# Kernel optimization log

Measured on AMD Instinct MI355X. Metric: run time of the kernel, lower is better.

Reference implementation:

```python
import jax, jax.numpy as jnp
import numpy as np

H, W, C = 128, 128, 100
N_OBJ = 3
PAD_VAL = 1e20  # WRONG_LABEL_PADDING-style padding used by local_pairwise_distances2


def setup_inputs() -> dict:
    key = jax.random.key(0)
    k1, k2, k3 = jax.random.split(key, 3)
    return {
        "prev_frame_embedding": jax.random.normal(k1, (H, W, C), dtype=jnp.float32),
        "query_embedding": jax.random.normal(k2, (H, W, C), dtype=jnp.float32),
        "prev_frame_labels": jax.random.randint(k3, (H, W, 1), 0, N_OBJ),
        "gt_ids": jnp.arange(N_OBJ),
        "max_distance": 15,
    }


def _local_nn_features(query_embedding, prev_frame_embedding, prev_frame_labels, gt_ids, max_distance):
    h, w, c = query_embedding.shape
    k = 2 * max_distance + 1  # static python int -> static shapes
    n_obj = gt_ids.shape[0]

    # masks: [h, w, n_obj] -- labels are [h, w, 1], broadcast against gt_ids
    masks = prev_frame_labels == gt_ids[None, None, :]

    # pad reference embedding with a huge value (matches torch F.pad value=1e20),
    # pad masks with False (matches torch zero padding)
    y_pad = jnp.pad(prev_frame_embedding,
                    ((max_distance, max_distance), (max_distance, max_distance), (0, 0)),
                    constant_values=PAD_VAL)
    m_pad = jnp.pad(masks,
                    ((max_distance, max_distance), (max_distance, max_distance), (0, 0)))

    # offsets in the same order as the torch nested loops (y_start outer, x_start inner)
    offs = jnp.stack(jnp.meshgrid(jnp.arange(k), jnp.arange(k), indexing="ij"), -1).reshape(-1, 2)

    x = query_embedding

    def per_offset(off):
        y_sl = jax.lax.dynamic_slice(y_pad, (off[0], off[1], 0), (h, w, c))
        m_sl = jax.lax.dynamic_slice(m_pad, (off[0], off[1], 0), (h, w, n_obj))
        diff = x - y_sl
        d = jnp.sum(diff * diff, axis=-1)  # [h, w]
        return d, m_sl

    # sequential map over the k*k window offsets keeps peak memory small
    d, offset_masks = jax.lax.map(per_offset, offs)  # [k2,h,w], [k2,h,w,n_obj]
    d = jnp.transpose(d, (1, 2, 0))                   # [h, w, k2]
    offset_masks = jnp.transpose(offset_masks, (1, 2, 0, 3))  # [h, w, k2, n_obj]

    # mask out wrong-object / out-of-frame offsets with distance 1.0 (torch pad=ones_like)
    d_masked = jnp.where(offset_masks, d[..., None], jnp.float32(1.0))
    dists = jnp.min(d_masked, axis=2)  # [h, w, n_obj]
    return dists.reshape(1, h, w, n_obj, 1)


def reference(prev_frame_embedding, query_embedding, prev_frame_labels, gt_ids, max_distance):
    return _local_nn_features(query_embedding, prev_frame_embedding,
                              prev_frame_labels, gt_ids, max_distance)
```

## Files before the change

kernel.cpp:

```cpp
#include <hip/hip_runtime.h>
#include <cstdint>


#define HW   128
#define NC   100
#define MD   15
#define NOBJ 3
#define PIX  (HW * HW)
#define NOUT (PIX * NOBJ)
#define PEN_NM (1 << 22)
#define CSENT  (1 << 28)
#define IINIT  (1 << 30)

typedef __attribute__((ext_vector_type(4))) int intx4;

__device__ inline intx4 quant_pack16(const float* v) {
    signed char b[16];
#pragma unroll
    for (int j = 0; j < 16; ++j) {
        int qi = __float2int_rn(v[j] * 32.f);
        b[j] = (signed char)max(-127, min(127, qi));
    }
    intx4 r;
#pragma unroll
    for (int w = 0; w < 4; ++w)
        r[w] = (b[4*w] & 255) | ((b[4*w+1] & 255) << 8) |
               ((b[4*w+2] & 255) << 16) | ((b[4*w+3] & 255) << 24);
    return r;
}

__global__ __launch_bounds__(256) void vos_prep(
    const float* __restrict__ P, const float* __restrict__ Q,
    const int* __restrict__ labels,
    signed char* __restrict__ Pq, signed char* __restrict__ Qa,
    int2* __restrict__ yl, float* __restrict__ x2)
{
    const int lane = threadIdx.x & 63;
    const int wid  = blockIdx.x * 4 + (threadIdx.x >> 6);

    if (wid < 2048) {
        const int pix = wid * 8 + (lane >> 3);
        const int col = pix & 127;
        const int c = lane & 7;
        const float* sp = P + (size_t)pix * NC;
        const int k0 = c * 16;
        float v[16];
#pragma unroll
        for (int c4 = 0; c4 < 4; ++c4) {
            float4 a = {0.f,0.f,0.f,0.f};
            if (k0 + c4 * 4 + 4 <= NC) a = *(const float4*)(sp + k0 + c4 * 4);
            v[c4*4+0]=a.x; v[c4*4+1]=a.y; v[c4*4+2]=a.z; v[c4*4+3]=a.w;
        }
        *(intx4*)(Pq + (size_t)pix * 128 + ((c ^ (col & 7)) << 4)) = quant_pack16(v);
        float part = 0.f;
#pragma unroll
        for (int j = 0; j < 16; ++j) part = fmaf(v[j], v[j], part);
        part += __shfl_xor(part, 1); part += __shfl_xor(part, 2); part += __shfl_xor(part, 4);
        if ((lane & 7) == 0)
            yl[pix] = make_int2(__float2int_rn(part * 512.f), labels[pix]);
    } else if (wid < 4096) {
        const int w2 = wid - 2048;
        const int row = w2 >> 4, rem = w2 & 15;
        const int tile = rem >> 1, kh = rem & 1;
        const int m = lane & 15, quad = lane >> 4;
        const int pix = row * HW + tile * 16 + m;
        const float* sp = Q + (size_t)pix * NC;
        const int k0 = kh * 64 + quad * 16;
        float v[16];
#pragma unroll
        for (int c4 = 0; c4 < 4; ++c4) {
            float4 a = {0.f,0.f,0.f,0.f};
            if (k0 + c4 * 4 + 4 <= NC) a = *(const float4*)(sp + k0 + c4 * 4);
            v[c4*4+0]=a.x; v[c4*4+1]=a.y; v[c4*4+2]=a.z; v[c4*4+3]=a.w;
        }
        *(intx4*)(Qa + ((size_t)((row*8 + tile)*2 + kh))*1024 + lane*16) = quant_pack16(v);
    } else {
        const int w3 = wid - 4096;
        const int pix = w3 * 8 + (lane >> 3);
        const int lp = lane & 7;
        const float* sp = Q + (size_t)pix * NC;
        float part = 0.f;
#pragma unroll
        for (int cc = 0; cc < 4; ++cc) {
            int k = lp * 16 + cc * 4;
            if (k <= 96) {
                float4 t = *(const float4*)(sp + k);
                part = fmaf(t.x,t.x,part); part = fmaf(t.y,t.y,part);
                part = fmaf(t.z,t.z,part); part = fmaf(t.w,t.w,part);
            }
        }
        part += __shfl_xor(part, 1); part += __shfl_xor(part, 2); part += __shfl_xor(part, 4);
        if (lp == 0) x2[pix] = part;
    }
}

__device__ inline void stage_row(const signed char* __restrict__ Pq,
                                 signed char* dst, int r, int wv, int lane) {
    const signed char* src = Pq + (size_t)r * 16384 + wv * 4096;
    signed char* d = dst + wv * 4096;
#pragma unroll
    for (int it = 0; it < 4; ++it)
        __builtin_amdgcn_global_load_lds(
            (const __attribute__((address_space(1))) unsigned int*)(src + it * 1024 + lane * 16),
            (__attribute__((address_space(3))) unsigned int*)(d + it * 1024), 16, 0, 0);
}

__global__ __launch_bounds__(256, 2) void vos_band(
    const signed char* __restrict__ Pq, const signed char* __restrict__ Qa,
    const int2* __restrict__ yl, const int* __restrict__ gt,
    float* __restrict__ part)
{
    __shared__ signed char Bs[2][2][16384];
    __shared__ int2 yl_s[4 * 128];

    const int tid  = threadIdx.x;
    const int lane = tid & 63;
    const int wv   = tid >> 6;
    const int quad = lane >> 4;
    const int n    = lane & 15;
    const int j0w  = wv * 32;

    const int b      = blockIdx.x;
    const int xcd    = b & 7;
    const int wi     = b >> 3;
    const int stripe = xcd * 8 + (wi & 7);
    const int ck     = wi >> 3;
    const int i0     = stripe * 2;
    const int rbase  = i0 - MD + ck * 4;
    const int rlo    = max(rbase, 0);
    const int rhi    = min(rbase + 4, HW);
    const int np     = (rhi > rlo) ? ((rhi - rlo + 1) >> 1) : 0;

    const int g0 = gt[0], g1 = gt[1], g2 = gt[2];

    if (np > 0) {
        stage_row(Pq, &Bs[0][0][0], rlo, wv, lane);
        if (rlo + 1 < rhi) stage_row(Pq, &Bs[0][1][0], rlo + 1, wv, lane);
    }

    for (int t = tid; t < 4 * 128; t += 256) {
        int rr = t >> 7, c = t & 127, r = rbase + rr;
        if ((unsigned)r < (unsigned)HW) yl_s[t] = yl[r * HW + c];
    }

    intx4 Af[2][2][2];
#pragma unroll
    for (int uc = 0; uc < 2; ++uc)
#pragma unroll
    for (int ur = 0; ur < 2; ++ur) {
        const signed char* bse = Qa + (size_t)((i0 + ur) * 8 + wv * 2 + uc) * 2048;
#pragma unroll
        for (int kh = 0; kh < 2; ++kh)
            Af[uc][ur][kh] = *(const intx4*)(bse + kh * 1024 + lane * 16);
    }

    bool bgt[4], blt[4];
#pragma unroll
    for (int reg = 0; reg < 4; ++reg) {
        int m = quad * 4 + reg;
        bgt[reg] = n > m;
        blt[reg] = n < m;
    }

    int mm[2][2][4][NOBJ];
#pragma unroll
    for (int uc = 0; uc < 2; ++uc)
#pragma unroll
    for (int ur = 0; ur < 2; ++ur)
#pragma unroll
    for (int reg = 0; reg < 4; ++reg) {
        mm[uc][ur][reg][0] = IINIT; mm[uc][ur][reg][1] = IINIT; mm[uc][ur][reg][2] = IINIT;
    }

    __syncthreads();

    for (int pi = 0; pi < np; ++pi) {
        const int ra = rlo + 2 * pi;
        const int rb = ra + 1;
        if (pi + 1 < np) {
            const int r2 = ra + 2;
            stage_row(Pq, &Bs[(pi + 1) & 1][0][0], r2, wv, lane);
            if (r2 + 1 < rhi) stage_row(Pq, &Bs[(pi + 1) & 1][1][0], r2 + 1, wv, lane);
        }

        const signed char* BA = &Bs[pi & 1][0][0];
        const signed char* BB = &Bs[pi & 1][1][0];
        const bool hasB = rb < rhi;
        bool rvA[2], rvB[2];
        rvA[0] = (unsigned)(ra - i0 + MD)     <= 2u * MD;
        rvA[1] = (unsigned)(ra - i0 - 1 + MD) <= 2u * MD;
        rvB[0] = hasB && ((unsigned)(rb - i0 + MD)     <= 2u * MD);
        rvB[1] = hasB && ((unsigned)(rb - i0 - 1 + MD) <= 2u * MD);
        const int rrA = (ra - rbase) * 128;
        const int rrB = (min(rb, rhi - 1) - rbase) * 128;

#pragma unroll
        for (int t = 0; t < 4; ++t) {
            const int base = j0w + 16 * (t - 1);
            if (base < 0 || base >= HW) continue;

            const int pcol = base + n;
            int2 ylA = yl_s[rrA + pcol];
            int2 ylB = yl_s[rrB + pcol];
            int pA0 = (ylA.y == g0) ? ylA.x : PEN_NM;
            int pA1 = (ylA.y == g1) ? ylA.x : PEN_NM;
            int pA2 = (ylA.y == g2) ? ylA.x : PEN_NM;
            int pB0 = (ylB.y == g0) ? ylB.x : PEN_NM;
            int pB1 = (ylB.y == g1) ? ylB.x : PEN_NM;
            int pB2 = (ylB.y == g2) ? ylB.x : PEN_NM;

            intx4 CA[2][2], CB[2][2];
#pragma unroll
            for (int uc = 0; uc < 2; ++uc)
#pragma unroll
            for (int ur = 0; ur < 2; ++ur) {
                CA[uc][ur] = (intx4){0,0,0,0};
                CB[uc][ur] = (intx4){0,0,0,0};
            }

#pragma unroll
            for (int kh = 0; kh < 2; ++kh) {
                const int off = pcol * 128 + (((kh * 4 + quad) ^ (pcol & 7)) << 4);
                intx4 bvA = *(const intx4*)(BA + off);
                intx4 bvB = *(const intx4*)(BB + off);
#pragma unroll
                for (int uc = 0; uc < 2; ++uc) {
                    if (uc == 0 && t == 3) continue;
                    if (uc == 1 && t == 0) continue;
#pragma unroll
                    for (int ur = 0; ur < 2; ++ur) {
                        CA[uc][ur] = __builtin_amdgcn_mfma_i32_16x16x64_i8(Af[uc][ur][kh], bvA, CA[uc][ur], 0, 0, 0);
                        CB[uc][ur] = __builtin_amdgcn_mfma_i32_16x16x64_i8(Af[uc][ur][kh], bvB, CB[uc][ur], 0, 0, 0);
                    }
                }
            }

#pragma unroll
            for (int uc = 0; uc < 2; ++uc) {
                if (uc == 0 && t == 3) continue;
                if (uc == 1 && t == 0) continue;
                const int du = t - 1 - uc;
#pragma unroll
                for (int ur = 0; ur < 2; ++ur) {
#pragma unroll
                    for (int reg = 0; reg < 4; ++reg) {
                        bool tri = (du == 0) | (du == -1 ? bgt[reg] : blt[reg]);
                        bool okA = rvA[ur] & tri;
                        bool okB = rvB[ur] & tri;
                        int cA = okA ? CA[uc][ur][reg] : -CSENT;
                        int cB = okB ? CB[uc][ur][reg] : -CSENT;
                        mm[uc][ur][reg][0] = min(min(mm[uc][ur][reg][0], pA0 - cA), pB0 - cB);
                        mm[uc][ur][reg][1] = min(min(mm[uc][ur][reg][1], pA1 - cA), pB1 - cB);
                        mm[uc][ur][reg][2] = min(min(mm[uc][ur][reg][2], pA2 - cA), pB2 - cB);
                    }
                }
            }
        }
        __syncthreads();
    }

#pragma unroll
    for (int s = 1; s < 16; s <<= 1) {
#pragma unroll
        for (int uc = 0; uc < 2; ++uc)
#pragma unroll
        for (int ur = 0; ur < 2; ++ur)
#pragma unroll
        for (int reg = 0; reg < 4; ++reg)
#pragma unroll
        for (int o = 0; o < NOBJ; ++o)
            mm[uc][ur][reg][o] = min(mm[uc][ur][reg][o], __shfl_xor(mm[uc][ur][reg][o], s));
    }

    float* ps = (float*)&Bs[0][0][0];
    if (n == 0) {
#pragma unroll
        for (int uc = 0; uc < 2; ++uc)
#pragma unroll
        for (int ur = 0; ur < 2; ++ur)
#pragma unroll
        for (int reg = 0; reg < 4; ++reg) {
            const int qcol = j0w + 16 * uc + quad * 4 + reg;
#pragma unroll
            for (int o = 0; o < NOBJ; ++o)
                ps[(ur * 128 + qcol) * 3 + o] = (float)mm[uc][ur][reg][o];
        }
    }
    __syncthreads();
    if (tid < 192) {
        float4 v = *(const float4*)(ps + tid * 4);
        *(float4*)(part + (size_t)ck * NOUT + i0 * 384 + tid * 4) = v;
    }
}

__global__ __launch_bounds__(256) void vos_combine(
    const float* __restrict__ part, const float* __restrict__ x2,
    float* __restrict__ out)
{
    const int t = blockIdx.x * 256 + threadIdx.x;
    float v = part[t];
#pragma unroll
    for (int ck = 1; ck < 8; ++ck) v = fminf(v, part[ck * NOUT + t]);
    v = v * (1.f / 512.f) + x2[t / 3];
    out[t] = fminf(fmaxf(v, 0.f), 1.0f);
}

extern "C" void kernel_launch(void* const* d_in, const int* in_sizes, int n_in,
                              void* d_out, int out_size, void* d_ws, size_t ws_size,
                              hipStream_t stream) {
    const float* P      = (const float*)d_in[0];
    const float* Q      = (const float*)d_in[1];
    const int*   labels = (const int*)d_in[2];
    const int*   gt     = (const int*)d_in[3];

    int2*  yl = (int2*)d_ws;
    float* x2 = (float*)(yl + PIX);
    signed char* Pq = (signed char*)(x2 + PIX);
    signed char* Qa = Pq + (size_t)PIX * 128;
    float* part = (float*)(Qa + (size_t)PIX * 128);
    float* out = (float*)d_out;

    vos_prep<<<1536, 256, 0, stream>>>(P, Q, labels, Pq, Qa, yl, x2);
    vos_band<<<512, 256, 0, stream>>>(Pq, Qa, yl, gt, part);
    vos_combine<<<NOUT / 256, 256, 0, stream>>>(part, x2, out);
}
```

Before: 87.76 us.

## Fuse combine into band kernel via ticket atomics and preload all band rows

```diff
diff --git a/kernel.cpp b/kernel.cpp
--- a/kernel.cpp
+++ b/kernel.cpp
@@ -33,10 +33,12 @@
     const float* __restrict__ P, const float* __restrict__ Q,
     const int* __restrict__ labels,
     signed char* __restrict__ Pq, signed char* __restrict__ Qa,
-    int2* __restrict__ yl, float* __restrict__ x2)
+    int2* __restrict__ yl, float* __restrict__ x2, int* __restrict__ ticket)
 {
     const int lane = threadIdx.x & 63;
     const int wid  = blockIdx.x * 4 + (threadIdx.x >> 6);
+
+    if (blockIdx.x == 0 && threadIdx.x < 64) ticket[threadIdx.x] = 0;
 
     if (wid < 2048) {
         const int pix = wid * 8 + (lane >> 3);
@@ -58,39 +60,30 @@
         part += __shfl_xor(part, 1); part += __shfl_xor(part, 2); part += __shfl_xor(part, 4);
         if ((lane & 7) == 0)
             yl[pix] = make_int2(__float2int_rn(part * 512.f), labels[pix]);
-    } else if (wid < 4096) {
+    } else {
         const int w2 = wid - 2048;
-        const int row = w2 >> 4, rem = w2 & 15;
-        const int tile = rem >> 1, kh = rem & 1;
+        const int row = w2 >> 3, tile = w2 & 7;
         const int m = lane & 15, quad = lane >> 4;
         const int pix = row * HW + tile * 16 + m;
         const float* sp = Q + (size_t)pix * NC;
-        const int k0 = kh * 64 + quad * 16;
-        float v[16];
-#pragma unroll
-        for (int c4 = 0; c4 < 4; ++c4) {
-            float4 a = {0.f,0.f,0.f,0.f};
-            if (k0 + c4 * 4 + 4 <= NC) a = *(const float4*)(sp + k0 + c4 * 4);
-            v[c4*4+0]=a.x; v[c4*4+1]=a.y; v[c4*4+2]=a.z; v[c4*4+3]=a.w;
-        }
-        *(intx4*)(Qa + ((size_t)((row*8 + tile)*2 + kh))*1024 + lane*16) = quant_pack16(v);
-    } else {
-        const int w3 = wid - 4096;
-        const int pix = w3 * 8 + (lane >> 3);
-        const int lp = lane & 7;
-        const float* sp = Q + (size_t)pix * NC;
-        float part = 0.f;
-#pragma unroll
-        for (int cc = 0; cc < 4; ++cc) {
-            int k = lp * 16 + cc * 4;
-            if (k <= 96) {
-                float4 t = *(const float4*)(sp + k);
-                part = fmaf(t.x,t.x,part); part = fmaf(t.y,t.y,part);
-                part = fmaf(t.z,t.z,part); part = fmaf(t.w,t.w,part);
+        signed char* dst = Qa + (size_t)((row * 8 + tile) * 2) * 1024 + lane * 16;
+        float x2p = 0.f;
+#pragma unroll
+        for (int kh = 0; kh < 2; ++kh) {
+            const int k0 = kh * 64 + quad * 16;
+            float v[16];
+#pragma unroll
+            for (int c4 = 0; c4 < 4; ++c4) {
+                float4 a = {0.f,0.f,0.f,0.f};
+                if (k0 + c4 * 4 + 4 <= NC) a = *(const float4*)(sp + k0 + c4 * 4);
+                v[c4*4+0]=a.x; v[c4*4+1]=a.y; v[c4*4+2]=a.z; v[c4*4+3]=a.w;
             }
-        }
-        part += __shfl_xor(part, 1); part += __shfl_xor(part, 2); part += __shfl_xor(part, 4);
-        if (lp == 0) x2[pix] = part;
+#pragma unroll
+            for (int j = 0; j < 16; ++j) x2p = fmaf(v[j], v[j], x2p);
+            *(intx4*)(dst + kh * 1024) = quant_pack16(v);
+        }
+        x2p += __shfl_xor(x2p, 16); x2p += __shfl_xor(x2p, 32);
+        if (quad == 0) x2[pix] = x2p;
     }
 }
 
@@ -108,10 +101,12 @@
 __global__ __launch_bounds__(256, 2) void vos_band(
     const signed char* __restrict__ Pq, const signed char* __restrict__ Qa,
     const int2* __restrict__ yl, const int* __restrict__ gt,
-    float* __restrict__ part)
+    const float* __restrict__ x2, float* __restrict__ part,
+    float* __restrict__ out, int* __restrict__ ticket)
 {
     __shared__ signed char Bs[2][2][16384];
     __shared__ int2 yl_s[4 * 128];
+    __shared__ int s_done;
 
     const int tid  = threadIdx.x;
     const int lane = tid & 63;
@@ -133,10 +128,8 @@
 
     const int g0 = gt[0], g1 = gt[1], g2 = gt[2];
 
-    if (np > 0) {
-        stage_row(Pq, &Bs[0][0][0], rlo, wv, lane);
-        if (rlo + 1 < rhi) stage_row(Pq, &Bs[0][1][0], rlo + 1, wv, lane);
-    }
+    for (int r = rlo; r < rhi; ++r)
+        stage_row(Pq, &Bs[(r - rlo) >> 1][(r - rlo) & 1][0], r, wv, lane);
 
     for (int t = tid; t < 4 * 128; t += 256) {
         int rr = t >> 7, c = t & 127, r = rbase + rr;
@@ -177,14 +170,8 @@
     for (int pi = 0; pi < np; ++pi) {
         const int ra = rlo + 2 * pi;
         const int rb = ra + 1;
-        if (pi + 1 < np) {
-            const int r2 = ra + 2;
-            stage_row(Pq, &Bs[(pi + 1) & 1][0][0], r2, wv, lane);
-            if (r2 + 1 < rhi) stage_row(Pq, &Bs[(pi + 1) & 1][1][0], r2 + 1, wv, lane);
-        }
-
-        const signed char* BA = &Bs[pi & 1][0][0];
-        const signed char* BB = &Bs[pi & 1][1][0];
+        const signed char* BA = &Bs[pi][0][0];
+        const signed char* BB = &Bs[pi][1][0];
         const bool hasB = rb < rhi;
         bool rvA[2], rvB[2];
         rvA[0] = (unsigned)(ra - i0 + MD)     <= 2u * MD;
@@ -256,7 +243,6 @@
                 }
             }
         }
-        __syncthreads();
     }
 
 #pragma unroll
@@ -272,6 +258,7 @@
             mm[uc][ur][reg][o] = min(mm[uc][ur][reg][o], __shfl_xor(mm[uc][ur][reg][o], s));
     }
 
+    __syncthreads();
     float* ps = (float*)&Bs[0][0][0];
     if (n == 0) {
 #pragma unroll
@@ -287,22 +274,27 @@
         }
     }
     __syncthreads();
+    const int obase = i0 * 384;
     if (tid < 192) {
         float4 v = *(const float4*)(ps + tid * 4);
-        *(float4*)(part + (size_t)ck * NOUT + i0 * 384 + tid * 4) = v;
-    }
-}
-
-__global__ __launch_bounds__(256) void vos_combine(
-    const float* __restrict__ part, const float* __restrict__ x2,
-    float* __restrict__ out)
-{
-    const int t = blockIdx.x * 256 + threadIdx.x;
-    float v = part[t];
-#pragma unroll
-    for (int ck = 1; ck < 8; ++ck) v = fminf(v, part[ck * NOUT + t]);
-    v = v * (1.f / 512.f) + x2[t / 3];
-    out[t] = fminf(fmaxf(v, 0.f), 1.0f);
+        *(float4*)(part + (size_t)ck * NOUT + obase + tid * 4) = v;
+    }
+
+    __threadfence();
+    __syncthreads();
+    if (tid == 0) s_done = atomicAdd(ticket + stripe, 1);
+    __syncthreads();
+    if (s_done == 7) {
+        __threadfence();
+        for (int v = tid; v < 768; v += 256) {
+            float mval = part[obase + v];
+#pragma unroll
+            for (int c2 = 1; c2 < 8; ++c2)
+                mval = fminf(mval, part[(size_t)c2 * NOUT + obase + v]);
+            float val = mval * (1.f / 512.f) + x2[(obase + v) / 3];
+            out[obase + v] = fminf(fmaxf(val, 0.f), 1.0f);
+        }
+    }
 }
 
 extern "C" void kernel_launch(void* const* d_in, const int* in_sizes, int n_in,
@@ -318,9 +310,9 @@
     signed char* Pq = (signed char*)(x2 + PIX);
     signed char* Qa = Pq + (size_t)PIX * 128;
     float* part = (float*)(Qa + (size_t)PIX * 128);
+    int* ticket = (int*)(part + (size_t)8 * NOUT);
     float* out = (float*)d_out;
 
-    vos_prep<<<1536, 256, 0, stream>>>(P, Q, labels, Pq, Qa, yl, x2);
-    vos_band<<<512, 256, 0, stream>>>(Pq, Qa, yl, gt, part);
-    vos_combine<<<NOUT / 256, 256, 0, stream>>>(part, x2, out);
-}
+    vos_prep<<<768, 256, 0, stream>>>(P, Q, labels, Pq, Qa, yl, x2, ticket);
+    vos_band<<<512, 256, 0, stream>>>(Pq, Qa, yl, gt, x2, part, out, ticket);
+}
```

Measured after the change: 123.9 us. 1.41x slower.
